# Kernel tuning notes

Hardware: AMD Instinct MI355X
Metric: run time of the kernel (lower is better)

The kernel has to match this reference:

```python
import jax, jax.numpy as jnp
import numpy as np

T, B, I, H = 512, 64, 512, 512

def _linear_init(key, out_dim, in_dim):
    # torch nn.Linear default init: U(-k, k), k = 1/sqrt(in_dim)
    k1, k2 = jax.random.split(key)
    bound = 1.0 / np.sqrt(in_dim)
    W = jax.random.uniform(k1, (out_dim, in_dim), jnp.float32, -bound, bound)
    b = jax.random.uniform(k2, (out_dim,), jnp.float32, -bound, bound)
    return W, b

def setup_inputs() -> dict:
    key = jax.random.key(0)
    ks = jax.random.split(key, 5)
    inputs = jax.random.normal(ks[0], (T, B, I), jnp.float32)
    Wf, bf = _linear_init(ks[1], H, I + H)
    Wi, bi = _linear_init(ks[2], H, I + H)
    Wg, bg = _linear_init(ks[3], H, I + H)
    Wo, bo = _linear_init(ks[4], H, I + H)
    return {"inputs": inputs, "Wf": Wf, "bf": bf, "Wi": Wi, "bi": bi,
            "Wg": Wg, "bg": bg, "Wo": Wo, "bo": bo}

def reference(inputs, Wf, bf, Wi, bi, Wg, bg, Wo, bo):
    hidden_dim = Wf.shape[0]
    batch = inputs.shape[1]
    h0 = jnp.zeros((batch, hidden_dim), inputs.dtype)
    c0 = jnp.zeros((batch, hidden_dim), inputs.dtype)

    def step(carry, x):
        hx, cx = carry
        comb = jnp.concatenate([x, hx], axis=1)        # [B, I+H]
        f = jax.nn.sigmoid(comb @ Wf.T + bf)
        i = jax.nn.sigmoid(comb @ Wi.T + bi)
        g = jnp.tanh(comb @ Wg.T + bg)
        o = jax.nn.sigmoid(comb @ Wo.T + bo)
        cx = f * cx + i * g
        hx = o * jnp.tanh(cx)
        return (hx, cx), hx

    (hx, cx), outputs = jax.lax.scan(step, (h0, c0), inputs)
    return outputs, hx, cx
```

## Files before the change

kernel.cpp:

```cpp
#include <hip/hip_runtime.h>
#include <hip/hip_bf16.h>
#include <stdint.h>
#include <stddef.h>


#define T_STEPS 512
#define BATCH   64
#define HDIM    512

using short8 = __attribute__((ext_vector_type(8))) short;
using f32x4  = __attribute__((ext_vector_type(4))) float;
using int4v  = __attribute__((ext_vector_type(4))) int;

__device__ __forceinline__ void gload_lds16(const void* g, void* l) {
  __builtin_amdgcn_global_load_lds((const __attribute__((address_space(1))) void*)g,
                                   (__attribute__((address_space(3))) void*)l, 16, 0, 0);
}
__device__ __forceinline__ float sigf(float x) { return 1.0f / (1.0f + __expf(-x)); }
__device__ __forceinline__ float tanh_fast(float x) {
  x = fminf(fmaxf(x, -15.0f), 15.0f);
  float e = __expf(2.0f * x);
  return (e - 1.0f) / (e + 1.0f);
}
__device__ __forceinline__ short bfb(float f) {
  __hip_bfloat16 h = __float2bfloat16(f);
  short s; __builtin_memcpy(&s, &h, 2); return s;
}
__device__ __forceinline__ unsigned bfbits(float f) {
  __hip_bfloat16 h = __float2bfloat16(f);
  unsigned short s; __builtin_memcpy(&s, &h, 2); return (unsigned)s;
}
__device__ __forceinline__ float bf2f(unsigned u) {
  return __builtin_bit_cast(float, u << 16);
}

__global__ __launch_bounds__(256) void k_prep(
    const float* __restrict__ Wf, const float* __restrict__ bf_,
    const float* __restrict__ Wi, const float* __restrict__ bi,
    const float* __restrict__ Wg, const float* __restrict__ bg,
    const float* __restrict__ Wo, const float* __restrict__ bo,
    __hip_bfloat16* __restrict__ wxbt, __hip_bfloat16* __restrict__ whbt,
    float* __restrict__ bias, __hip_bfloat16* __restrict__ hbuf, int* __restrict__ flags)
{
  int idx = blockIdx.x * 256 + threadIdx.x;
  int row = idx >> 9;
  int k   = idx & 511;
  int g = row >> 9, r = row & 511;
  const float* W = (g == 0) ? Wf : (g == 1) ? Wi : (g == 2) ? Wg : Wo;
  const float* B = (g == 0) ? bf_ : (g == 1) ? bi : (g == 2) ? bg : bo;
  wxbt[(size_t)row * 512 + k] = __float2bfloat16(W[(size_t)r * 1024 + k]);
  whbt[(size_t)row * 512 + k] = __float2bfloat16(W[(size_t)r * 1024 + 512 + k]);
  if (k == 0) bias[row] = B[r];
  if (idx < 2 * BATCH * HDIM) hbuf[idx] = __float2bfloat16(0.0f);
  if (idx < 128) flags[idx] = 0;
}

__global__ __launch_bounds__(256) void k_convx(const float* __restrict__ x,
                                               __hip_bfloat16* __restrict__ xbf)
{
  int idx = blockIdx.x * 256 + threadIdx.x;
  const float4* p = (const float4*)x + (size_t)idx * 2;
  float4 a = p[0], b = p[1];
  short8 o;
  o[0]=bfb(a.x); o[1]=bfb(a.y); o[2]=bfb(a.z); o[3]=bfb(a.w);
  o[4]=bfb(b.x); o[5]=bfb(b.y); o[6]=bfb(b.z); o[7]=bfb(b.w);
  *(short8*)((short*)xbf + (size_t)idx * 8) = o;
}

__global__ __launch_bounds__(256) void k_xproj(
    const __hip_bfloat16* __restrict__ xbf,
    const __hip_bfloat16* __restrict__ wxbt,
    const float* __restrict__ bias,
    __hip_bfloat16* __restrict__ xproj)
{
  __shared__ __align__(16) short aT[128 * 64];
  __shared__ __align__(16) short bT[128 * 64];
  const int tid = threadIdx.x, lane = tid & 63, wave = tid >> 6;
  const int m0 = blockIdx.y * 128, n0 = blockIdx.x * 128;
  const int wr = wave >> 1, wc = wave & 1;

  f32x4 acc[4][4] = {};

  for (int s = 0; s < 8; ++s) {
    __syncthreads();
    const int kbyte = s * 128;
#pragma unroll
    for (int it = 0; it < 4; ++it) {
      int flat = it * 256 + tid;
      int row = flat >> 3, gr = flat & 7;
      int sgr = gr ^ (row & 7);
      const char* ga = (const char*)xbf  + (size_t)(m0 + row) * 1024 + kbyte + sgr * 16;
      const char* gb = (const char*)wxbt + (size_t)(n0 + row) * 1024 + kbyte + sgr * 16;
      gload_lds16(ga, (char*)aT + (it * 256 + wave * 64) * 16);
      gload_lds16(gb, (char*)bT + (it * 256 + wave * 64) * 16);
    }
    __syncthreads();
#pragma unroll
    for (int kk2 = 0; kk2 < 2; ++kk2) {
      short8 af[4], bfr[4];
#pragma unroll
      for (int mt = 0; mt < 4; ++mt) {
        int r = wr * 64 + mt * 16 + (lane & 15);
        int g = (kk2 * 4 + (lane >> 4)) ^ (r & 7);
        af[mt] = *(const short8*)((const char*)aT + r * 128 + g * 16);
      }
#pragma unroll
      for (int nt = 0; nt < 4; ++nt) {
        int r = wc * 64 + nt * 16 + (lane & 15);
        int g = (kk2 * 4 + (lane >> 4)) ^ (r & 7);
        bfr[nt] = *(const short8*)((const char*)bT + r * 128 + g * 16);
      }
#pragma unroll
      for (int mt = 0; mt < 4; ++mt)
#pragma unroll
        for (int nt = 0; nt < 4; ++nt)
          acc[mt][nt] = __builtin_amdgcn_mfma_f32_16x16x32_bf16(af[mt], bfr[nt], acc[mt][nt], 0, 0, 0);
    }
  }
#pragma unroll
  for (int nt = 0; nt < 4; ++nt) {
    int n = n0 + wc * 64 + nt * 16 + (lane & 15);
    float bv = bias[n];
    int j2 = (n >> 4) & 31, g2 = n >> 9, c2 = n & 15;
#pragma unroll
    for (int mt = 0; mt < 4; ++mt)
#pragma unroll
      for (int i = 0; i < 4; ++i) {
        int m = m0 + wr * 64 + mt * 16 + (lane >> 4) * 4 + i;
        int tt = m >> 6, rr = m & 63;
        xproj[(((size_t)tt * 32 + j2) * 64 + rr) * 64 + g2 * 16 + c2] =
            __float2bfloat16(acc[mt][nt][i] + bv);
      }
  }
}

__global__ __launch_bounds__(64, 1) void k_recur(
    const __hip_bfloat16* __restrict__ xproj,
    const __hip_bfloat16* __restrict__ whbt,
    __hip_bfloat16* __restrict__ hbuf,
    float* __restrict__ out,
    int* __restrict__ flags)
{
  const int lane = threadIdx.x;
  const int bid  = blockIdx.x;
  const int j = bid >> 2, w = bid & 3;
  const int hc0 = j * 16, col = lane & 15, q = lane >> 4, mrow = q * 4;

  float c_state[4] = {0.f, 0.f, 0.f, 0.f};
  float* out_hx = out + (size_t)T_STEPS * BATCH * HDIM;
  float* out_cx = out_hx + BATCH * HDIM;

  const char* wbase = (const char*)whbt + ((size_t)(hc0 + col)) * 1024 + q * 16;

  for (int t = 0; t < T_STEPS; ++t) {
    const int cur = t & 1;
    short8 bw[16][4];
#pragma unroll
    for (int kk = 0; kk < 16; ++kk)
#pragma unroll
      for (int gg = 0; gg < 4; ++gg)
        bw[kk][gg] = *(const short8*)(wbase + (size_t)gg * 524288 + (size_t)kk * 64);

    const char* xpb = (const char*)xproj +
        (((size_t)t * 32 + j) * 4096 + (size_t)(w * 16 + mrow) * 64 + col) * 2;
    unsigned xpu[4][4];
#pragma unroll
    for (int g = 0; g < 4; ++g)
#pragma unroll
      for (int i = 0; i < 4; ++i) {
        const void* p = xpb + i * 128 + g * 32;
        asm volatile("global_load_ushort %0, %1, off"
                     : "=v"(xpu[g][i]) : "v"(p) : "memory");
      }
    if (t > 0) {
      const int* fp = flags + w * 32 + (lane & 31);
      int f0, f1;
      asm volatile("global_load_dword %0, %1, off sc0 sc1" : "=v"(f0) : "v"(fp) : "memory");
      asm volatile("s_waitcnt vmcnt(0)" ::: "memory");
      if (f0 < t) {
        for (;;) {
          asm volatile("global_load_dword %0, %1, off sc0 sc1" : "=v"(f1) : "v"(fp) : "memory");
          asm volatile("s_waitcnt vmcnt(1)" ::: "memory");
          if (f0 >= t) break;
          asm volatile("global_load_dword %0, %1, off sc0 sc1" : "=v"(f0) : "v"(fp) : "memory");
          asm volatile("s_waitcnt vmcnt(1)" ::: "memory");
          if (f1 >= t) break;
        }
        asm volatile("s_waitcnt vmcnt(0)" ::: "memory");
      }
    } else {
      asm volatile("s_waitcnt vmcnt(0)" ::: "memory");
    }

    const char* hb = (const char*)hbuf + cur * (BATCH * HDIM * 2) +
                     (size_t)(w * 16 + (lane & 15)) * 1024 + q * 16;
    int4v araw[16];
#pragma unroll
    for (int kk = 0; kk < 16; ++kk) {
      const void* p = hb + kk * 64;
      asm volatile("global_load_dwordx4 %0, %1, off sc0 sc1"
                   : "=v"(araw[kk]) : "v"(p) : "memory");
    }
    f32x4 acc[4] = {};
#pragma unroll
    for (int kk = 0; kk < 16; ++kk) {
      asm volatile("s_waitcnt vmcnt(%0)" :: "i"(15 - kk) : "memory");
      __builtin_amdgcn_sched_barrier(0);
      short8 af = __builtin_bit_cast(short8, araw[kk]);
#pragma unroll
      for (int gg = 0; gg < 4; ++gg)
        acc[gg] = __builtin_amdgcn_mfma_f32_16x16x32_bf16(af, bw[kk][gg], acc[gg], 0, 0, 0);
    }

    float hnv[4], cnv[4];
#pragma unroll
    for (int i = 0; i < 4; ++i) {
      float pf = acc[0][i] + bf2f(xpu[0][i]);
      float pi = acc[1][i] + bf2f(xpu[1][i]);
      float pg = acc[2][i] + bf2f(xpu[2][i]);
      float po = acc[3][i] + bf2f(xpu[3][i]);
      float fg = sigf(pf), ig = sigf(pi), gg2 = tanh_fast(pg), og = sigf(po);
      float cn = fg * c_state[i] + ig * gg2;
      c_state[i] = cn;
      cnv[i] = cn;
      hnv[i] = og * tanh_fast(cn);
    }
    char* hnxt = (char*)hbuf + (cur ^ 1) * (BATCH * HDIM * 2) +
                 ((size_t)(w * 16 + mrow) * 512 + hc0 + col) * 2;
#pragma unroll
    for (int i = 0; i < 4; ++i) {
      unsigned hb16 = bfbits(hnv[i]);
      void* p = hnxt + i * 1024;
      asm volatile("global_store_short %0, %1, off sc0 sc1"
                   :: "v"(p), "v"(hb16) : "memory");
    }
    asm volatile("s_waitcnt vmcnt(0)" ::: "memory");
    if (t < T_STEPS - 1 && lane == 0) {
      int nv = t + 1;
      int* fp2 = flags + w * 32 + j;
      asm volatile("global_store_dword %0, %1, off sc0 sc1"
                   :: "v"(fp2), "v"(nv) : "memory");
    }
    float* outb = out + ((size_t)t * BATCH + w * 16 + mrow) * HDIM + hc0 + col;
#pragma unroll
    for (int i = 0; i < 4; ++i) outb[(size_t)i * HDIM] = hnv[i];
    if (t == T_STEPS - 1) {
#pragma unroll
      for (int i = 0; i < 4; ++i) {
        out_hx[(size_t)(w * 16 + mrow + i) * HDIM + hc0 + col] = hnv[i];
        out_cx[(size_t)(w * 16 + mrow + i) * HDIM + hc0 + col] = cnv[i];
      }
    }
  }
}

extern "C" void kernel_launch(void* const* d_in, const int* in_sizes, int n_in,
                              void* d_out, int out_size, void* d_ws, size_t ws_size,
                              hipStream_t stream) {
  const float* x   = (const float*)d_in[0];
  const float* Wf  = (const float*)d_in[1];
  const float* bf_ = (const float*)d_in[2];
  const float* Wi  = (const float*)d_in[3];
  const float* bi  = (const float*)d_in[4];
  const float* Wg  = (const float*)d_in[5];
  const float* bg  = (const float*)d_in[6];
  const float* Wo  = (const float*)d_in[7];
  const float* bo  = (const float*)d_in[8];

  char* ws = (char*)d_ws;
  __hip_bfloat16* xbf   = (__hip_bfloat16*)(ws);
  __hip_bfloat16* wxbt  = (__hip_bfloat16*)(ws + 33554432);
  __hip_bfloat16* whbt  = (__hip_bfloat16*)(ws + 35651584);
  float*          bias  = (float*)         (ws + 37748736);
  __hip_bfloat16* xproj = (__hip_bfloat16*)(ws + 37756928);
  __hip_bfloat16* hbuf  = (__hip_bfloat16*)(ws + 171974656);
  int*            flags = (int*)           (ws + 172105728);

  k_prep <<<4096, 256, 0, stream>>>(Wf, bf_, Wi, bi, Wg, bg, Wo, bo,
                                    wxbt, whbt, bias, hbuf, flags);
  k_convx<<<8192, 256, 0, stream>>>(x, xbf);
  k_xproj<<<dim3(16, 256), 256, 0, stream>>>(xbf, wxbt, bias, xproj);
  k_recur<<<128, 64, 0, stream>>>(xproj, whbt, hbuf, (float*)d_out, flags);
}
```

Before: 1.691 ms.

## Tag hidden-state words with step number to validate data without waiting on flags

Stores each bf16 hidden value in a 32-bit word whose upper half carries the timestep tag. Readers load h optimistically and check the tags per k-chunk, retrying only the chunks that are stale. The store no longer waits on vmcnt(0) before writing the flag. The intent is to take the flag-then-load round trip and the store-drain wait off the recurrent critical path. In exchange the h buffer and its load traffic double, the retry path adds code, and the flag polling still appears to remain.

```diff
diff --git a/kernel.cpp b/kernel.cpp
--- a/kernel.cpp
+++ b/kernel.cpp
@@ -32,6 +32,14 @@
 }
 __device__ __forceinline__ float bf2f(unsigned u) {
   return __builtin_bit_cast(float, u << 16);
+}
+__device__ __forceinline__ short8 unpack_pair(int4v r0, int4v r1) {
+  int4v afw;
+  afw[0] = (r0[0] & 0xffff) | (r0[1] << 16);
+  afw[1] = (r0[2] & 0xffff) | (r0[3] << 16);
+  afw[2] = (r1[0] & 0xffff) | (r1[1] << 16);
+  afw[3] = (r1[2] & 0xffff) | (r1[3] << 16);
+  return __builtin_bit_cast(short8, afw);
 }
 
 __global__ __launch_bounds__(256) void k_prep(
@@ -40,7 +48,7 @@
     const float* __restrict__ Wg, const float* __restrict__ bg,
     const float* __restrict__ Wo, const float* __restrict__ bo,
     __hip_bfloat16* __restrict__ wxbt, __hip_bfloat16* __restrict__ whbt,
-    float* __restrict__ bias, __hip_bfloat16* __restrict__ hbuf, int* __restrict__ flags)
+    float* __restrict__ bias, unsigned* __restrict__ hbuf32, int* __restrict__ flags)
 {
   int idx = blockIdx.x * 256 + threadIdx.x;
   int row = idx >> 9;
@@ -51,7 +59,7 @@
   wxbt[(size_t)row * 512 + k] = __float2bfloat16(W[(size_t)r * 1024 + k]);
   whbt[(size_t)row * 512 + k] = __float2bfloat16(W[(size_t)r * 1024 + 512 + k]);
   if (k == 0) bias[row] = B[r];
-  if (idx < 2 * BATCH * HDIM) hbuf[idx] = __float2bfloat16(0.0f);
+  if (idx < 2 * BATCH * HDIM) hbuf32[idx] = 0u;
   if (idx < 128) flags[idx] = 0;
 }
 
@@ -137,7 +145,7 @@
 __global__ __launch_bounds__(64, 1) void k_recur(
     const __hip_bfloat16* __restrict__ xproj,
     const __hip_bfloat16* __restrict__ whbt,
-    __hip_bfloat16* __restrict__ hbuf,
+    unsigned* __restrict__ hbuf32,
     float* __restrict__ out,
     int* __restrict__ flags)
 {
@@ -151,6 +159,8 @@
   float* out_cx = out_hx + BATCH * HDIM;
 
   const char* wbase = (const char*)whbt + ((size_t)(hc0 + col)) * 1024 + q * 16;
+  const char* hbl = (const char*)hbuf32 +
+                    ((size_t)(w * 16 + (lane & 15)) * 512 + q * 8) * 4;
 
   for (int t = 0; t < T_STEPS; ++t) {
     const int cur = t & 1;
@@ -192,24 +202,66 @@
       asm volatile("s_waitcnt vmcnt(0)" ::: "memory");
     }
 
-    const char* hb = (const char*)hbuf + cur * (BATCH * HDIM * 2) +
-                     (size_t)(w * 16 + (lane & 15)) * 1024 + q * 16;
-    int4v araw[16];
+    const char* hb = hbl + (size_t)cur * (BATCH * HDIM * 4);
+    int4v raw[32];
+#pragma unroll
+    for (int ii = 0; ii < 32; ++ii) {
+      const void* p = hb + (size_t)(ii >> 1) * 128 + (ii & 1) * 16;
+      asm volatile("global_load_dwordx4 %0, %1, off sc0 sc1"
+                   : "=v"(raw[ii]) : "v"(p) : "memory");
+    }
+    f32x4 acc[4] = {};
+    unsigned bad = 0u;
 #pragma unroll
     for (int kk = 0; kk < 16; ++kk) {
-      const void* p = hb + kk * 64;
-      asm volatile("global_load_dwordx4 %0, %1, off sc0 sc1"
-                   : "=v"(araw[kk]) : "v"(p) : "memory");
-    }
-    f32x4 acc[4] = {};
-#pragma unroll
-    for (int kk = 0; kk < 16; ++kk) {
-      asm volatile("s_waitcnt vmcnt(%0)" :: "i"(15 - kk) : "memory");
+      asm volatile("s_waitcnt vmcnt(%0)" :: "i"(30 - 2 * kk) : "memory");
       __builtin_amdgcn_sched_barrier(0);
-      short8 af = __builtin_bit_cast(short8, araw[kk]);
-#pragma unroll
-      for (int gg = 0; gg < 4; ++gg)
-        acc[gg] = __builtin_amdgcn_mfma_f32_16x16x32_bf16(af, bw[kk][gg], acc[gg], 0, 0, 0);
+      unsigned a = (unsigned)raw[2*kk][0]   & (unsigned)raw[2*kk][1]
+                 & (unsigned)raw[2*kk][2]   & (unsigned)raw[2*kk][3]
+                 & (unsigned)raw[2*kk+1][0] & (unsigned)raw[2*kk+1][1]
+                 & (unsigned)raw[2*kk+1][2] & (unsigned)raw[2*kk+1][3];
+      if (__builtin_expect(__all((a >> 16) == (unsigned)t), 1)) {
+        short8 af = unpack_pair(raw[2*kk], raw[2*kk+1]);
+#pragma unroll
+        for (int gg = 0; gg < 4; ++gg)
+          acc[gg] = __builtin_amdgcn_mfma_f32_16x16x32_bf16(af, bw[kk][gg], acc[gg], 0, 0, 0);
+      } else {
+        bad |= 1u << kk;
+      }
+    }
+    if (__builtin_expect(bad != 0u, 0)) {
+      while (bad) {
+        unsigned still = 0u;
+#pragma unroll
+        for (int kk = 0; kk < 16; ++kk)
+          if (bad & (1u << kk)) {
+            const void* p0 = hb + (size_t)kk * 256;
+            const void* p1 = hb + (size_t)kk * 256 + 16;
+            asm volatile("global_load_dwordx4 %0, %1, off sc0 sc1"
+                         : "=v"(raw[2*kk]) : "v"(p0) : "memory");
+            asm volatile("global_load_dwordx4 %0, %1, off sc0 sc1"
+                         : "=v"(raw[2*kk+1]) : "v"(p1) : "memory");
+          }
+        asm volatile("s_waitcnt vmcnt(0)" ::: "memory");
+        __builtin_amdgcn_sched_barrier(0);
+#pragma unroll
+        for (int kk = 0; kk < 16; ++kk)
+          if (bad & (1u << kk)) {
+            unsigned a = (unsigned)raw[2*kk][0]   & (unsigned)raw[2*kk][1]
+                       & (unsigned)raw[2*kk][2]   & (unsigned)raw[2*kk][3]
+                       & (unsigned)raw[2*kk+1][0] & (unsigned)raw[2*kk+1][1]
+                       & (unsigned)raw[2*kk+1][2] & (unsigned)raw[2*kk+1][3];
+            if (__all((a >> 16) == (unsigned)t)) {
+              short8 af = unpack_pair(raw[2*kk], raw[2*kk+1]);
+#pragma unroll
+              for (int gg = 0; gg < 4; ++gg)
+                acc[gg] = __builtin_amdgcn_mfma_f32_16x16x32_bf16(af, bw[kk][gg], acc[gg], 0, 0, 0);
+            } else {
+              still |= 1u << kk;
+            }
+          }
+        bad = still;
+      }
     }
 
     float hnv[4], cnv[4];
@@ -225,21 +277,23 @@
       cnv[i] = cn;
       hnv[i] = og * tanh_fast(cn);
     }
-    char* hnxt = (char*)hbuf + (cur ^ 1) * (BATCH * HDIM * 2) +
-                 ((size_t)(w * 16 + mrow) * 512 + hc0 + col) * 2;
-#pragma unroll
-    for (int i = 0; i < 4; ++i) {
-      unsigned hb16 = bfbits(hnv[i]);
-      void* p = hnxt + i * 1024;
-      asm volatile("global_store_short %0, %1, off sc0 sc1"
-                   :: "v"(p), "v"(hb16) : "memory");
-    }
-    asm volatile("s_waitcnt vmcnt(0)" ::: "memory");
-    if (t < T_STEPS - 1 && lane == 0) {
-      int nv = t + 1;
-      int* fp2 = flags + w * 32 + j;
-      asm volatile("global_store_dword %0, %1, off sc0 sc1"
-                   :: "v"(fp2), "v"(nv) : "memory");
+    if (t < T_STEPS - 1) {
+      char* hnxt = (char*)hbuf32 + (size_t)(cur ^ 1) * (BATCH * HDIM * 4) +
+                   ((size_t)(w * 16 + mrow) * 512 + hc0 + col) * 4;
+      unsigned tag = ((unsigned)(t + 1)) << 16;
+#pragma unroll
+      for (int i = 0; i < 4; ++i) {
+        unsigned word = bfbits(hnv[i]) | tag;
+        void* p = hnxt + (size_t)i * 2048;
+        asm volatile("global_store_dword %0, %1, off sc0 sc1"
+                     :: "v"(p), "v"(word) : "memory");
+      }
+      if (lane == 0) {
+        int nv = t + 1;
+        int* fp2 = flags + w * 32 + j;
+        asm volatile("global_store_dword %0, %1, off sc0 sc1"
+                     :: "v"(fp2), "v"(nv) : "memory");
+      }
     }
     float* outb = out + ((size_t)t * BATCH + w * 16 + mrow) * HDIM + hc0 + col;
 #pragma unroll
@@ -273,12 +327,12 @@
   __hip_bfloat16* whbt  = (__hip_bfloat16*)(ws + 35651584);
   float*          bias  = (float*)         (ws + 37748736);
   __hip_bfloat16* xproj = (__hip_bfloat16*)(ws + 37756928);
-  __hip_bfloat16* hbuf  = (__hip_bfloat16*)(ws + 171974656);
-  int*            flags = (int*)           (ws + 172105728);
+  unsigned*       hbuf32= (unsigned*)      (ws + 171974656);
+  int*            flags = (int*)           (ws + 172236800);
 
   k_prep <<<4096, 256, 0, stream>>>(Wf, bf_, Wi, bi, Wg, bg, Wo, bo,
-                                    wxbt, whbt, bias, hbuf, flags);
+                                    wxbt, whbt, bias, hbuf32, flags);
   k_convx<<<8192, 256, 0, stream>>>(x, xbf);
   k_xproj<<<dim3(16, 256), 256, 0, stream>>>(xbf, wxbt, bias, xproj);
-  k_recur<<<128, 64, 0, stream>>>(xproj, whbt, hbuf, (float*)d_out, flags);
-}
+  k_recur<<<128, 64, 0, stream>>>(xproj, whbt, hbuf32, (float*)d_out, flags);
+}
```

New measurement: 2.292 ms. 1.36x slower.

## Share h-state loads across four waves via LDS and vectorize xproj loads

Applied to the files above, without the earlier changes.

The recurrent kernel now runs 32 blocks of 256 threads instead of 128 single-wave blocks. Each block has four waves that share one batch slice. The waves load the previous h tile from global memory cooperatively into a swizzled LDS buffer, and each wave reads its MFMA A operands from LDS. Only wave 0 polls the inter-block flags, and a block barrier releases the rest. The xproj layout is permuted so each lane fetches its 16 gate pre-activations with two 16-byte loads instead of 16 short loads. The goal is to cut redundant global traffic and per-step latency, at the cost of two __syncthreads per timestep.

```diff
diff --git a/kernel.cpp b/kernel.cpp
--- a/kernel.cpp
+++ b/kernel.cpp
@@ -125,25 +125,27 @@
 #pragma unroll
     for (int mt = 0; mt < 4; ++mt)
 #pragma unroll
-      for (int i = 0; i < 4; ++i) {
-        int m = m0 + wr * 64 + mt * 16 + (lane >> 4) * 4 + i;
+      for (int i2 = 0; i2 < 4; ++i2) {
+        int m = m0 + wr * 64 + mt * 16 + (lane >> 4) * 4 + i2;
         int tt = m >> 6, rr = m & 63;
-        xproj[(((size_t)tt * 32 + j2) * 64 + rr) * 64 + g2 * 16 + c2] =
-            __float2bfloat16(acc[mt][nt][i] + bv);
+        int w2 = rr >> 4, q2 = (rr >> 2) & 3, ii = rr & 3;
+        size_t off = ((((size_t)tt * 32 + j2) * 4 + w2) * 4 + q2) * 16 + c2;
+        xproj[off * 16 + g2 * 4 + ii] = __float2bfloat16(acc[mt][nt][i2] + bv);
       }
   }
 }
 
-__global__ __launch_bounds__(64, 1) void k_recur(
+__global__ __launch_bounds__(256, 1) void k_recur(
     const __hip_bfloat16* __restrict__ xproj,
     const __hip_bfloat16* __restrict__ whbt,
     __hip_bfloat16* __restrict__ hbuf,
     float* __restrict__ out,
     int* __restrict__ flags)
 {
-  const int lane = threadIdx.x;
-  const int bid  = blockIdx.x;
-  const int j = bid >> 2, w = bid & 3;
+  __shared__ __align__(16) short hlds[16 * 512];
+  const int tid = threadIdx.x, lane = tid & 63, wave = tid >> 6;
+  const int b = blockIdx.x;
+  const int w = b & 3, j = (b >> 2) * 4 + wave;
   const int hc0 = j * 16, col = lane & 15, q = lane >> 4, mrow = q * 4;
 
   float c_state[4] = {0.f, 0.f, 0.f, 0.f};
@@ -151,6 +153,8 @@
   float* out_cx = out_hx + BATCH * HDIM;
 
   const char* wbase = (const char*)whbt + ((size_t)(hc0 + col)) * 1024 + q * 16;
+  const char* lrow = (const char*)hlds + (size_t)col * 1024;
+  const int   swz  = col & 7;
 
   for (int t = 0; t < T_STEPS; ++t) {
     const int cur = t & 1;
@@ -162,17 +166,11 @@
         bw[kk][gg] = *(const short8*)(wbase + (size_t)gg * 524288 + (size_t)kk * 64);
 
     const char* xpb = (const char*)xproj +
-        (((size_t)t * 32 + j) * 4096 + (size_t)(w * 16 + mrow) * 64 + col) * 2;
-    unsigned xpu[4][4];
-#pragma unroll
-    for (int g = 0; g < 4; ++g)
-#pragma unroll
-      for (int i = 0; i < 4; ++i) {
-        const void* p = xpb + i * 128 + g * 32;
-        asm volatile("global_load_ushort %0, %1, off"
-                     : "=v"(xpu[g][i]) : "v"(p) : "memory");
-      }
-    if (t > 0) {
+        (((((size_t)t * 32 + j) * 4 + w) * 4 + q) * 16 + col) * 32;
+    int4v xw0 = *(const int4v*)xpb;
+    int4v xw1 = *(const int4v*)(xpb + 16);
+
+    if (wave == 0 && t > 0) {
       const int* fp = flags + w * 32 + (lane & 31);
       int f0, f1;
       asm volatile("global_load_dword %0, %1, off sc0 sc1" : "=v"(f0) : "v"(fp) : "memory");
@@ -188,25 +186,32 @@
         }
         asm volatile("s_waitcnt vmcnt(0)" ::: "memory");
       }
-    } else {
-      asm volatile("s_waitcnt vmcnt(0)" ::: "memory");
-    }
-
-    const char* hb = (const char*)hbuf + cur * (BATCH * HDIM * 2) +
-                     (size_t)(w * 16 + (lane & 15)) * 1024 + q * 16;
-    int4v araw[16];
+    }
+    __syncthreads();
+
+    const char* hgb = (const char*)hbuf + cur * (BATCH * HDIM * 2) +
+                      (size_t)(w * 16 + col) * 1024;
+    int4v hv[4];
+#pragma unroll
+    for (int s = 0; s < 4; ++s) {
+      const void* p = hgb + (size_t)(wave * 16 + s * 4 + q) * 16;
+      asm volatile("global_load_dwordx4 %0, %1, off sc0 sc1"
+                   : "=v"(hv[s]) : "v"(p) : "memory");
+    }
+    asm volatile("s_waitcnt vmcnt(0)" ::: "memory");
+    __builtin_amdgcn_sched_barrier(0);
+#pragma unroll
+    for (int s = 0; s < 4; ++s) {
+      int g0 = wave * 16 + s * 4 + q;
+      *(int4v*)((char*)lrow + ((g0 ^ swz) << 4)) = hv[s];
+    }
+    __syncthreads();
+
+    f32x4 acc[4] = {};
 #pragma unroll
     for (int kk = 0; kk < 16; ++kk) {
-      const void* p = hb + kk * 64;
-      asm volatile("global_load_dwordx4 %0, %1, off sc0 sc1"
-                   : "=v"(araw[kk]) : "v"(p) : "memory");
-    }
-    f32x4 acc[4] = {};
-#pragma unroll
-    for (int kk = 0; kk < 16; ++kk) {
-      asm volatile("s_waitcnt vmcnt(%0)" :: "i"(15 - kk) : "memory");
-      __builtin_amdgcn_sched_barrier(0);
-      short8 af = __builtin_bit_cast(short8, araw[kk]);
+      int g0 = (kk * 4 + q) ^ swz;
+      short8 af = *(const short8*)(lrow + (g0 << 4));
 #pragma unroll
       for (int gg = 0; gg < 4; ++gg)
         acc[gg] = __builtin_amdgcn_mfma_f32_16x16x32_bf16(af, bw[kk][gg], acc[gg], 0, 0, 0);
@@ -215,11 +220,15 @@
     float hnv[4], cnv[4];
 #pragma unroll
     for (int i = 0; i < 4; ++i) {
-      float pf = acc[0][i] + bf2f(xpu[0][i]);
-      float pi = acc[1][i] + bf2f(xpu[1][i]);
-      float pg = acc[2][i] + bf2f(xpu[2][i]);
-      float po = acc[3][i] + bf2f(xpu[3][i]);
-      float fg = sigf(pf), ig = sigf(pi), gg2 = tanh_fast(pg), og = sigf(po);
+      float pv[4];
+#pragma unroll
+      for (int g = 0; g < 4; ++g) {
+        int idx = g * 4 + i, wd = idx >> 1;
+        unsigned v = (unsigned)(wd < 4 ? xw0[wd] : xw1[wd - 4]);
+        unsigned u = (idx & 1) ? (v >> 16) : (v & 0xffffu);
+        pv[g] = acc[g][i] + bf2f(u);
+      }
+      float fg = sigf(pv[0]), ig = sigf(pv[1]), gg2 = tanh_fast(pv[2]), og = sigf(pv[3]);
       float cn = fg * c_state[i] + ig * gg2;
       c_state[i] = cn;
       cnv[i] = cn;
@@ -280,5 +289,5 @@
                                     wxbt, whbt, bias, hbuf, flags);
   k_convx<<<8192, 256, 0, stream>>>(x, xbf);
   k_xproj<<<dim3(16, 256), 256, 0, stream>>>(xbf, wxbt, bias, xproj);
-  k_recur<<<128, 64, 0, stream>>>(xproj, whbt, hbuf, (float*)d_out, flags);
-}
+  k_recur<<<32, 256, 0, stream>>>(xproj, whbt, hbuf, (float*)d_out, flags);
+}
```

New measurement: 1.974 ms. 1.17x slower.

## Vectorize xproj loads via per-lane layout and prefetch sync flags early

Applied to the files above, without the earlier changes.

The projection GEMM epilogue now writes xproj in a lane-contiguous layout, so each recurrent lane fetches its 16 gate preactivations with two 16-byte loads instead of 16 scalar ushort loads. The flag polling skips each block's own flag. It also prefetches the flag value right after publishing its own flag, so the spin loop is entered only when the prefetched value is stale. The aim is to cut per-step latency on the serial critical path of the recurrence. The trade-off is a tighter layout coupling between the two kernels and a possibly stale prefetched flag, which falls back to polling.

```diff
diff --git a/kernel.cpp b/kernel.cpp
--- a/kernel.cpp
+++ b/kernel.cpp
@@ -125,11 +125,12 @@
 #pragma unroll
     for (int mt = 0; mt < 4; ++mt)
 #pragma unroll
-      for (int i = 0; i < 4; ++i) {
-        int m = m0 + wr * 64 + mt * 16 + (lane >> 4) * 4 + i;
+      for (int i2 = 0; i2 < 4; ++i2) {
+        int m = m0 + wr * 64 + mt * 16 + (lane >> 4) * 4 + i2;
         int tt = m >> 6, rr = m & 63;
-        xproj[(((size_t)tt * 32 + j2) * 64 + rr) * 64 + g2 * 16 + c2] =
-            __float2bfloat16(acc[mt][nt][i] + bv);
+        int w2 = rr >> 4, q2 = (rr >> 2) & 3, ii = rr & 3;
+        size_t off = ((((size_t)tt * 32 + j2) * 4 + w2) * 4 + q2) * 16 + c2;
+        xproj[off * 16 + g2 * 4 + ii] = __float2bfloat16(acc[mt][nt][i2] + bv);
       }
   }
 }
@@ -145,12 +146,16 @@
   const int bid  = blockIdx.x;
   const int j = bid >> 2, w = bid & 3;
   const int hc0 = j * 16, col = lane & 15, q = lane >> 4, mrow = q * 4;
+  const bool need = (lane & 31) != j;
 
   float c_state[4] = {0.f, 0.f, 0.f, 0.f};
   float* out_hx = out + (size_t)T_STEPS * BATCH * HDIM;
   float* out_cx = out_hx + BATCH * HDIM;
 
   const char* wbase = (const char*)whbt + ((size_t)(hc0 + col)) * 1024 + q * 16;
+  const int* fp = flags + w * 32 + (lane & 31);
+
+  int f0pre = 0;
 
   for (int t = 0; t < T_STEPS; ++t) {
     const int cur = t & 1;
@@ -162,18 +167,13 @@
         bw[kk][gg] = *(const short8*)(wbase + (size_t)gg * 524288 + (size_t)kk * 64);
 
     const char* xpb = (const char*)xproj +
-        (((size_t)t * 32 + j) * 4096 + (size_t)(w * 16 + mrow) * 64 + col) * 2;
-    unsigned xpu[4][4];
-#pragma unroll
-    for (int g = 0; g < 4; ++g)
-#pragma unroll
-      for (int i = 0; i < 4; ++i) {
-        const void* p = xpb + i * 128 + g * 32;
-        asm volatile("global_load_ushort %0, %1, off"
-                     : "=v"(xpu[g][i]) : "v"(p) : "memory");
-      }
-    if (t > 0) {
-      const int* fp = flags + w * 32 + (lane & 31);
+        (((((size_t)t * 32 + j) * 4 + w) * 4 + q) * 16 + col) * 32;
+    int4v xw0 = *(const int4v*)xpb;
+    int4v xw1 = *(const int4v*)(xpb + 16);
+
+    asm volatile("s_waitcnt vmcnt(0)" ::: "memory");
+    __builtin_amdgcn_sched_barrier(0);
+    if (t > 0 && need && f0pre < t) {
       int f0, f1;
       asm volatile("global_load_dword %0, %1, off sc0 sc1" : "=v"(f0) : "v"(fp) : "memory");
       asm volatile("s_waitcnt vmcnt(0)" ::: "memory");
@@ -188,9 +188,8 @@
         }
         asm volatile("s_waitcnt vmcnt(0)" ::: "memory");
       }
-    } else {
-      asm volatile("s_waitcnt vmcnt(0)" ::: "memory");
-    }
+    }
+    __builtin_amdgcn_sched_barrier(0);
 
     const char* hb = (const char*)hbuf + cur * (BATCH * HDIM * 2) +
                      (size_t)(w * 16 + (lane & 15)) * 1024 + q * 16;
@@ -215,11 +214,15 @@
     float hnv[4], cnv[4];
 #pragma unroll
     for (int i = 0; i < 4; ++i) {
-      float pf = acc[0][i] + bf2f(xpu[0][i]);
-      float pi = acc[1][i] + bf2f(xpu[1][i]);
-      float pg = acc[2][i] + bf2f(xpu[2][i]);
-      float po = acc[3][i] + bf2f(xpu[3][i]);
-      float fg = sigf(pf), ig = sigf(pi), gg2 = tanh_fast(pg), og = sigf(po);
+      float pv[4];
+#pragma unroll
+      for (int g = 0; g < 4; ++g) {
+        int idx = g * 4 + i, wd = idx >> 1;
+        unsigned v = (unsigned)(wd < 4 ? xw0[wd] : xw1[wd - 4]);
+        unsigned u = (idx & 1) ? (v >> 16) : (v & 0xffffu);
+        pv[g] = acc[g][i] + bf2f(u);
+      }
+      float fg = sigf(pv[0]), ig = sigf(pv[1]), gg2 = tanh_fast(pv[2]), og = sigf(pv[3]);
       float cn = fg * c_state[i] + ig * gg2;
       c_state[i] = cn;
       cnv[i] = cn;
@@ -235,11 +238,15 @@
                    :: "v"(p), "v"(hb16) : "memory");
     }
     asm volatile("s_waitcnt vmcnt(0)" ::: "memory");
-    if (t < T_STEPS - 1 && lane == 0) {
-      int nv = t + 1;
-      int* fp2 = flags + w * 32 + j;
-      asm volatile("global_store_dword %0, %1, off sc0 sc1"
-                   :: "v"(fp2), "v"(nv) : "memory");
+    if (t < T_STEPS - 1) {
+      if (lane == 0) {
+        int nv = t + 1;
+        int* fp2 = flags + w * 32 + j;
+        asm volatile("global_store_dword %0, %1, off sc0 sc1"
+                     :: "v"(fp2), "v"(nv) : "memory");
+      }
+      asm volatile("global_load_dword %0, %1, off sc0 sc1"
+                   : "=v"(f0pre) : "v"(fp) : "memory");
     }
     float* outb = out + ((size_t)t * BATCH + w * 16 + mrow) * HDIM + hc0 + col;
 #pragma unroll
```

After: 1.654 ms. 2.2% less time.
